# Performance work log

Measured on AMD Instinct MI355X. Metric: run time of the kernel, lower is better.

## Reference

```python
import jax, jax.numpy as jnp
import numpy as np

EPS_ANGLE = 1e-8   # eps in _cos_angle's F.normalize
EPS_NORM = 1e-12   # default F.normalize eps used for the similarity matrix
TOPK = 4
EXTRA_FRAMES = (1, 3, 5, 7)          # teacher-only frames
SHARED_TEACHER = (2, 4, 6)           # shared frames in teacher indexing
SHARED_STUDENT = (1, 2, 3)           # same frames in student indexing
W1 = W2 = W3 = 1.0


def _angle_cosines(ref, shared, sim):
    """Cosines of the 3 RKD angles for every (ref r, shared s, sim k) triplet.
    ref: [B,R,D], shared: [B,S,D], sim: [B,R,K,D]. Returns 3 arrays [B,R,S,K].
    Uses the dot-product expansion (u-v).(w-v) = uw - uv - vw + vv so the
    [B,R,S,K,D] difference tensors are never materialized (same math as the
    chunked torch loop)."""
    rr = jnp.sum(ref * ref, -1)                       # [B,R]
    ss = jnp.sum(shared * shared, -1)                 # [B,S]
    hh = jnp.sum(sim * sim, -1)                       # [B,R,K]
    sr = jnp.einsum('brd,bsd->brs', ref, shared)      # [B,R,S]
    rh = jnp.einsum('brd,brkd->brk', ref, sim)        # [B,R,K]
    sh = jnp.einsum('bsd,brkd->brsk', shared, sim)    # [B,R,S,K]
    rr_ = rr[:, :, None, None]
    ss_ = ss[:, None, :, None]
    hh_ = hh[:, :, None, :]
    sr_ = sr[..., None]
    rh_ = rh[:, :, None, :]
    n_sr = jnp.sqrt(jnp.maximum(ss_ - 2 * sr_ + rr_, 0.0))  # ||shared-ref||
    n_hr = jnp.sqrt(jnp.maximum(hh_ - 2 * rh_ + rr_, 0.0))  # ||sim-ref||
    n_sh = jnp.sqrt(jnp.maximum(ss_ - 2 * sh + hh_, 0.0))   # ||shared-sim||
    cl = lambda n: jnp.maximum(n, EPS_ANGLE)
    a1 = (sh - rh_ - sr_ + rr_) / (cl(n_sr) * cl(n_hr))  # angle at ref
    a2 = (sr_ - sh - rh_ + hh_) / (cl(n_hr) * cl(n_sh))  # angle at sim
    a3 = (rh_ - sr_ - sh + ss_) / (cl(n_sr) * cl(n_sh))  # angle at shared
    return a1, a2, a3


def _l2n(x, eps):
    return x / jnp.maximum(jnp.linalg.norm(x, axis=-1, keepdims=True), eps)


def setup_inputs() -> dict:
    key = jax.random.key(0)
    k1, k2, k3, k4 = jax.random.split(key, 4)
    B, P, D = 4, 1024, 1024
    return {
        'teacher_feats': jax.random.normal(k1, (B, 8, P, D), dtype=jnp.float32),
        'student_feats': jax.random.normal(k2, (B, 4, P, D), dtype=jnp.float32),
        'ref_perm': jax.random.randint(k3, (256,), 0, P),
        'shared_perm': jax.random.randint(k4, (256,), 0, P),
    }


def reference(teacher_feats, student_feats, ref_perm, shared_perm):
    B, St, P, D = teacher_feats.shape
    R = ref_perm.shape[0]
    S = shared_perm.shape[0]
    sg = jax.lax.stop_gradient

    ref_t = sg(teacher_feats[:, 0, ref_perm, :])        # [B,R,D]
    ref_s = student_feats[:, 0, ref_perm, :]            # [B,R,D]

    # teacher-only (extra) frames, concatenated along patch dim -> [B,4P,D]
    extra_t = sg(teacher_feats[:, jnp.array(EXTRA_FRAMES), :, :]).reshape(B, len(EXTRA_FRAMES) * P, D)
    sim = jnp.einsum('brd,bed->bre', _l2n(ref_t, EPS_NORM), _l2n(extra_t, EPS_NORM))
    _, topk_idx = jax.lax.top_k(sim, TOPK)              # [B,R,K]
    sim_high = jax.vmap(lambda e, i: e[i])(extra_t, topk_idx)  # [B,R,K,D]
    sim_high = sg(sim_high)

    s1 = s2 = s3 = jnp.float32(0.0)
    for ti, si in zip(SHARED_TEACHER, SHARED_STUDENT):
        sh_t = sg(teacher_feats[:, ti, shared_perm, :])
        sh_s = student_feats[:, si, shared_perm, :]
        a1t, a2t, a3t = _angle_cosines(ref_t, sh_t, sim_high)
        a1s, a2s, a3s = _angle_cosines(ref_s, sh_s, sim_high)
        s1 = s1 + jnp.sum(jnp.abs(a1s - sg(a1t)))
        s2 = s2 + jnp.sum(jnp.abs(a2s - sg(a2t)))
        s3 = s3 + jnp.sum(jnp.abs(a3s - sg(a3t)))

    total_elements = len(SHARED_TEACHER) * B * R * S * TOPK
    loss = (W1 * s1 + W2 * s2 + W3 * s3) / total_elements
    return loss
```

## Files before the change

kernel.cpp:

```cpp
#include <hip/hip_runtime.h>
#include <float.h>

#define BB 4
#define PP 1024
#define DD 1024
#define RR 256
#define SSZ 256
#define KT 4
#define EE 4096
#define NPAIR 3

typedef float  f32x4  __attribute__((ext_vector_type(4)));
typedef short  short8 __attribute__((ext_vector_type(8)));

#define MFMA16(a,b,c) __builtin_amdgcn_mfma_f32_16x16x32_bf16((a),(b),(c),0,0,0)

#define OFF_NE    ((size_t)0)
#define OFF_RR_T  ((size_t)16384)
#define OFF_RR_S  ((size_t)17408)
#define OFF_HH    ((size_t)18432)
#define OFF_RH_T  ((size_t)22528)
#define OFF_RH_S  ((size_t)26624)
#define OFF_SS_T  ((size_t)30720)
#define OFF_SS_S  ((size_t)33792)
#define OFF_TOPK  ((size_t)36864)
#define OFF_ACC   ((size_t)40960)
#define OFF_CAND  ((size_t)45056)
#define FLOAT_END ((size_t)569344)

#define U_REF_T ((size_t)0)
#define U_REF_S ((size_t)2097152)
#define U_SIMH  ((size_t)4194304)
#define U_SH_T  ((size_t)8388608)
#define U_SH_S  ((size_t)11534336)
#define U_EXT   ((size_t)14680064)

__device__ inline float block_sum256(float v, float* sb) {
  v += __shfl_down(v, 32); v += __shfl_down(v, 16);
  v += __shfl_down(v, 8);  v += __shfl_down(v, 4);
  v += __shfl_down(v, 2);  v += __shfl_down(v, 1);
  int lane = threadIdx.x & 63, wid = threadIdx.x >> 6;
  if (lane == 0) sb[wid] = v;
  __syncthreads();
  float r = 0.f;
  if (threadIdx.x < 4) r = sb[threadIdx.x];
  r += __shfl_down(r, 2); r += __shfl_down(r, 1);
  __syncthreads();
  return r;
}

__device__ inline float dot4(const float4& a, const float4& b) {
  return a.x*b.x + a.y*b.y + a.z*b.z + a.w*b.w;
}

__device__ inline unsigned short bhi(float x) {
  unsigned u = __float_as_uint(x);
  return (unsigned short)((u + 0x7fffu + ((u >> 16) & 1u)) >> 16);
}
__device__ inline ushort4 h4of(float4 f) {
  return make_ushort4(bhi(f.x), bhi(f.y), bhi(f.z), bhi(f.w));
}

__device__ inline size_t wofs(size_t base, int R, int t) {
  int rr = R & 15;
  int ss = ((t >> 1) & 3) ^ ((rr >> 1) & 3);
  return base + (size_t)(R >> 4)*16384 + (size_t)(t >> 3)*512
       + rr*32 + ss*8 + (t & 1)*4;
}

__global__ __launch_bounds__(256) void k_prep(const float* __restrict__ T,
                                              const float* __restrict__ Sf,
                                              const int* __restrict__ ref_perm,
                                              const int* __restrict__ shared_perm,
                                              float* __restrict__ ws) {
  __shared__ float sb[4];
  ushort* uws = (ushort*)(ws + FLOAT_END);
  int blk = blockIdx.x;
  int t = threadIdx.x;
  if (blk < 1024) {
    int b = blk >> 8, r = blk & 255;
    int pos = ref_perm[r];
    const float4* ts = (const float4*)(T  + ((size_t)(b*8 + 0)*PP + pos)*DD);
    const float4* sv = (const float4*)(Sf + ((size_t)(b*4 + 0)*PP + pos)*DD);
    float4 a = ts[t], c = sv[t];
    int R = b*RR + r;
    *(ushort4*)(uws + wofs(U_REF_T, R, t)) = h4of(a);
    *(ushort4*)(uws + wofs(U_REF_S, R, t)) = h4of(c);
    float r1 = block_sum256(dot4(a, a), sb);
    float r2 = block_sum256(dot4(c, c), sb);
    if (t == 0) {
      ws[OFF_RR_T + R] = r1;
      ws[OFF_RR_S + R] = r2;
    }
  } else if (blk < 17408) {
    int i = blk - 1024;
    int b = i >> 12, e = i & 4095;
    int f = 1 + 2*(e >> 10);
    int pos = e & 1023;
    const float4* src = (const float4*)(T + ((size_t)(b*8 + f)*PP + pos)*DD);
    float4 a = src[t];
    *(ushort4*)(uws + wofs(U_EXT, b*EE + e, t)) = h4of(a);
    float tot = block_sum256(dot4(a, a), sb);
    if (t == 0) ws[OFF_NE + (size_t)b*EE + e] = fmaxf(sqrtf(tot), 1e-12f);
  } else {
    int idx = blk - 17408;
    int p = idx / (BB*SSZ);
    int b = (idx / SSZ) % BB;
    int s = idx % SSZ;
    int pos = shared_perm[s];
    int ti = 2*(p + 1), si = p + 1;
    const float4* tr = (const float4*)(T  + ((size_t)(b*8 + ti)*PP + pos)*DD);
    const float4* sr = (const float4*)(Sf + ((size_t)(b*4 + si)*PP + pos)*DD);
    float4 a = tr[t], c = sr[t];
    *(ushort4*)(uws + wofs(U_SH_T, idx, t)) = h4of(a);
    *(ushort4*)(uws + wofs(U_SH_S, idx, t)) = h4of(c);
    float r1 = block_sum256(dot4(a, a), sb);
    float r2 = block_sum256(dot4(c, c), sb);
    if (t == 0) { ws[OFF_SS_T + idx] = r1; ws[OFF_SS_S + idx] = r2; }
  }
}

__global__ __launch_bounds__(256) void k_sim(float* __restrict__ ws) {
  __shared__ float simv[4][16][68];
  const ushort* uws = (const ushort*)(ws + FLOAT_END);
  int d = blockIdx.x;
  int u8 = d & 7, q = d >> 3;
  int b = u8 >> 1, eh = u8 & 1;
  int eb = eh*32 + (q >> 2);
  int rgq = q & 3;
  int tid = threadIdx.x;
  int w = tid >> 6, lane = tid & 63;
  int rg = rgq*4 + w;
  int r0 = rg*16, e0 = eb*64;
  int l15 = lane & 15, lq = (lane >> 4) & 3;
  int laneoff = l15*32 + ((lq ^ ((l15 >> 1) & 3)))*8;

  const ushort* pA = uws + U_REF_T + ((size_t)((b*RR + r0) >> 4))*16384 + laneoff;
  const ushort* pB0 = uws + U_EXT + ((size_t)((b*EE + e0) >> 4) + 0)*16384 + laneoff;
  const ushort* pB1 = uws + U_EXT + ((size_t)((b*EE + e0) >> 4) + 1)*16384 + laneoff;
  const ushort* pB2 = uws + U_EXT + ((size_t)((b*EE + e0) >> 4) + 2)*16384 + laneoff;
  const ushort* pB3 = uws + U_EXT + ((size_t)((b*EE + e0) >> 4) + 3)*16384 + laneoff;

  f32x4 acc[4];
#pragma unroll
  for (int j = 0; j < 4; ++j) acc[j] = (f32x4){0.f, 0.f, 0.f, 0.f};

#pragma unroll 4
  for (int c = 0; c < 32; ++c) {
    int o = c*512;
    short8 ah = *(const short8*)(pA + o);
    short8 b0 = *(const short8*)(pB0 + o);
    short8 b1 = *(const short8*)(pB1 + o);
    short8 b2 = *(const short8*)(pB2 + o);
    short8 b3 = *(const short8*)(pB3 + o);
    acc[0] = MFMA16(ah, b0, acc[0]);
    acc[1] = MFMA16(ah, b1, acc[1]);
    acc[2] = MFMA16(ah, b2, acc[2]);
    acc[3] = MFMA16(ah, b3, acc[3]);
  }

  float invs[4];
#pragma unroll
  for (int j = 0; j < 4; ++j)
    invs[j] = 1.f / ws[OFF_NE + (size_t)b*EE + e0 + j*16 + l15];
#pragma unroll
  for (int j = 0; j < 4; ++j)
#pragma unroll
    for (int q2 = 0; q2 < 4; ++q2)
      simv[w][lq*4 + q2][j*16 + l15] = acc[j][q2] * invs[j];
  if (lane < 16) {
    float v[4] = {-FLT_MAX, -FLT_MAX, -FLT_MAX, -FLT_MAX};
    int ix[4] = {0x7fffffff, 0x7fffffff, 0x7fffffff, 0x7fffffff};
#pragma unroll 1
    for (int e = 0; e < 64; ++e) {
      float f = simv[w][lane][e];
      if (f > v[3]) {
        int eg = e0 + e;
        if (f > v[0])      { v[3]=v[2]; ix[3]=ix[2]; v[2]=v[1]; ix[2]=ix[1]; v[1]=v[0]; ix[1]=ix[0]; v[0]=f; ix[0]=eg; }
        else if (f > v[1]) { v[3]=v[2]; ix[3]=ix[2]; v[2]=v[1]; ix[2]=ix[1]; v[1]=f; ix[1]=eg; }
        else if (f > v[2]) { v[3]=v[2]; ix[3]=ix[2]; v[2]=f; ix[2]=eg; }
        else               { v[3]=f; ix[3]=eg; }
      }
    }
    float2* cand = (float2*)(ws + OFF_CAND);
    size_t base = (((size_t)(b*RR + r0 + lane))*64 + eb)*4;
#pragma unroll
    for (int k = 0; k < 4; ++k)
      cand[base + k] = make_float2(v[k], __int_as_float(ix[k]));
  }
}

__global__ __launch_bounds__(256) void k_topk2(float* __restrict__ ws) {
  __shared__ float rv[256];
  __shared__ int   ri[256];
  __shared__ int   winIdx;
  int br = blockIdx.x;
  int tid = threadIdx.x;
  const float2* cand = (const float2*)(ws + OFF_CAND);
  float2 c = cand[(size_t)br*256 + tid];
  float v = c.x;
  int idx = __float_as_int(c.y);
  int* outi = (int*)(ws + OFF_TOPK) + (size_t)br*KT;
  for (int k = 0; k < KT; ++k) {
    rv[tid] = v; ri[tid] = idx;
    __syncthreads();
    for (int off = 128; off > 0; off >>= 1) {
      if (tid < off) {
        float v2 = rv[tid+off]; int i2 = ri[tid+off];
        if (v2 > rv[tid] || (v2 == rv[tid] && i2 < ri[tid])) { rv[tid] = v2; ri[tid] = i2; }
      }
      __syncthreads();
    }
    if (tid == 0) { outi[k] = ri[0]; winIdx = ri[0]; }
    __syncthreads();
    if (idx == winIdx) v = -FLT_MAX;
    __syncthreads();
  }
}

__global__ __launch_bounds__(256) void k_gather_high(const float* __restrict__ T,
                                                     const float* __restrict__ Sf,
                                                     const int* __restrict__ ref_perm,
                                                     float* __restrict__ ws) {
  __shared__ float sb[4];
  int idx = blockIdx.x;
  int e = ((const int*)(ws + OFF_TOPK))[idx];
  int b = idx >> 10;
  int r = (idx >> 2) & 255;
  int rpos = ref_perm[r];
  const float4* src = (const float4*)(T + ((size_t)(b*8 + 1 + 2*(e >> 10))*PP + (e & 1023))*DD);
  const float4* rt  = (const float4*)(T  + ((size_t)(b*8 + 0)*PP + rpos)*DD);
  const float4* rs  = (const float4*)(Sf + ((size_t)(b*4 + 0)*PP + rpos)*DD);
  ushort* uws = (ushort*)(ws + FLOAT_END);
  int t = threadIdx.x;
  float4 h = src[t];
  *(ushort4*)(uws + wofs(U_SIMH, idx, t)) = h4of(h);
  float4 a = rt[t], c = rs[t];
  float r1 = block_sum256(dot4(h, h), sb);
  float r2 = block_sum256(dot4(h, a), sb);
  float r3 = block_sum256(dot4(h, c), sb);
  if (t == 0) { ws[OFF_HH + idx] = r1; ws[OFF_RH_T + idx] = r2; ws[OFF_RH_S + idx] = r3; }
}

__global__ __launch_bounds__(256) void k_main(float* __restrict__ ws,
                                              double* __restrict__ acc_out) {
  __shared__ float Ct[4][80][17];
  __shared__ float Cs2[4][80][17];
  __shared__ float sb[4];
  const ushort* uws = (const ushort*)(ws + FLOAT_END);

  int d = blockIdx.x;
  int u8 = d & 7, q = d >> 3;
  int b = u8 >> 1, rhalf = u8 & 1;
  int p = q >> 4;
  int rem = q & 15;
  int s32i = rem >> 1, rq = rem & 1;
  int tid = threadIdx.x;
  int w = tid >> 6, lane = tid & 63;
  int z = p*4 + b;
  int r16i = rhalf*8 + rq*4 + w;
  int r0 = r16i*16, s0 = s32i*32;

  int l15 = lane & 15, lq = (lane >> 4) & 3;
  int laneoff = l15*32 + ((lq ^ ((l15 >> 1) & 3)))*8;

  const ushort* pa0; const ushort* pa1; const ushort* pa2; const ushort* pa3;
  const ushort* prt; const ushort* prs;
  const ushort* pbt0; const ushort* pbt1; const ushort* pbs0; const ushort* pbs1;
  {
    size_t gs = (size_t)((b*RR + r0) >> 2);
    pa0 = uws + U_SIMH + (gs + 0)*16384 + laneoff;
    pa1 = uws + U_SIMH + (gs + 1)*16384 + laneoff;
    pa2 = uws + U_SIMH + (gs + 2)*16384 + laneoff;
    pa3 = uws + U_SIMH + (gs + 3)*16384 + laneoff;
    size_t gr = (size_t)((b*RR + r0) >> 4);
    prt = uws + U_REF_T + gr*16384 + laneoff;
    prs = uws + U_REF_S + gr*16384 + laneoff;
    size_t gh = (size_t)((z*SSZ + s0) >> 4);
    pbt0 = uws + U_SH_T + (gh + 0)*16384 + laneoff;
    pbt1 = uws + U_SH_T + (gh + 1)*16384 + laneoff;
    pbs0 = uws + U_SH_S + (gh + 0)*16384 + laneoff;
    pbs1 = uws + U_SH_S + (gh + 1)*16384 + laneoff;
  }

  f32x4 aT0[2], aT1[2], aT2[2], aT3[2], aRT[2];
  f32x4 aS0[2], aS1[2], aS2[2], aS3[2], aRS[2];
#pragma unroll
  for (int h = 0; h < 2; ++h) {
    aT0[h] = aT1[h] = aT2[h] = aT3[h] = aRT[h] = (f32x4){0.f,0.f,0.f,0.f};
    aS0[h] = aS1[h] = aS2[h] = aS3[h] = aRS[h] = (f32x4){0.f,0.f,0.f,0.f};
  }

#pragma unroll 2
  for (int c = 0; c < 32; ++c) {
    int o = c*512;
    short8 bt0 = *(const short8*)(pbt0 + o);
    short8 bt1 = *(const short8*)(pbt1 + o);
    short8 bs0 = *(const short8*)(pbs0 + o);
    short8 bs1 = *(const short8*)(pbs1 + o);
    short8 a0 = *(const short8*)(pa0 + o);
    short8 a1 = *(const short8*)(pa1 + o);
    short8 a2 = *(const short8*)(pa2 + o);
    short8 a3 = *(const short8*)(pa3 + o);
    short8 rt = *(const short8*)(prt + o);
    short8 rs = *(const short8*)(prs + o);
    aT0[0] = MFMA16(a0, bt0, aT0[0]);  aT0[1] = MFMA16(a0, bt1, aT0[1]);
    aT1[0] = MFMA16(a1, bt0, aT1[0]);  aT1[1] = MFMA16(a1, bt1, aT1[1]);
    aT2[0] = MFMA16(a2, bt0, aT2[0]);  aT2[1] = MFMA16(a2, bt1, aT2[1]);
    aT3[0] = MFMA16(a3, bt0, aT3[0]);  aT3[1] = MFMA16(a3, bt1, aT3[1]);
    aRT[0] = MFMA16(rt, bt0, aRT[0]);  aRT[1] = MFMA16(rt, bt1, aRT[1]);
    aS0[0] = MFMA16(a0, bs0, aS0[0]);  aS0[1] = MFMA16(a0, bs1, aS0[1]);
    aS1[0] = MFMA16(a1, bs0, aS1[0]);  aS1[1] = MFMA16(a1, bs1, aS1[1]);
    aS2[0] = MFMA16(a2, bs0, aS2[0]);  aS2[1] = MFMA16(a2, bs1, aS2[1]);
    aS3[0] = MFMA16(a3, bs0, aS3[0]);  aS3[1] = MFMA16(a3, bs1, aS3[1]);
    aRS[0] = MFMA16(rs, bs0, aRS[0]);  aRS[1] = MFMA16(rs, bs1, aRS[1]);
  }

  int rl = lane >> 2, sg = lane & 3;
  int r = r0 + rl;
  float rrt = ws[OFF_RR_T + b*RR + r];
  float rrs = ws[OFF_RR_S + b*RR + r];
  float hhk[4], rhtk[4], rhsk[4], ihr_t[4], ihr_s[4];
#pragma unroll
  for (int k = 0; k < 4; ++k) {
    int idx = (b*RR + r)*KT + k;
    hhk[k]  = ws[OFF_HH + idx];
    rhtk[k] = ws[OFF_RH_T + idx];
    rhsk[k] = ws[OFF_RH_S + idx];
    float nt = sqrtf(fmaxf(hhk[k] - 2.f*rhtk[k] + rrt, 0.f));
    float ns = sqrtf(fmaxf(hhk[k] - 2.f*rhsk[k] + rrs, 0.f));
    ihr_t[k] = 1.f / fmaxf(nt, 1e-8f);
    ihr_s[k] = 1.f / fmaxf(ns, 1e-8f);
  }

  float local = 0.f;
#pragma unroll
  for (int h = 0; h < 2; ++h) {
#pragma unroll
    for (int q2 = 0; q2 < 4; ++q2) {
      int rg = lq*4 + q2;
      Ct[w][ 0 + rg][l15] = aT0[h][q2];
      Ct[w][16 + rg][l15] = aT1[h][q2];
      Ct[w][32 + rg][l15] = aT2[h][q2];
      Ct[w][48 + rg][l15] = aT3[h][q2];
      Ct[w][64 + rg][l15] = aRT[h][q2];
      Cs2[w][ 0 + rg][l15] = aS0[h][q2];
      Cs2[w][16 + rg][l15] = aS1[h][q2];
      Cs2[w][32 + rg][l15] = aS2[h][q2];
      Cs2[w][48 + rg][l15] = aS3[h][q2];
      Cs2[w][64 + rg][l15] = aRS[h][q2];
    }
#pragma unroll
    for (int j = 0; j < 4; ++j) {
      int sl = sg*4 + j;
      int sidx = z*SSZ + s0 + h*16 + sl;
      float sst = ws[OFF_SS_T + sidx];
      float sss = ws[OFF_SS_S + sidx];
      float srt = Ct[w][64 + rl][sl];
      float srs = Cs2[w][64 + rl][sl];
      float isr_t = 1.f / fmaxf(sqrtf(fmaxf(sst - 2.f*srt + rrt, 0.f)), 1e-8f);
      float isr_s = 1.f / fmaxf(sqrtf(fmaxf(sss - 2.f*srs + rrs, 0.f)), 1e-8f);
#pragma unroll
      for (int k = 0; k < 4; ++k) {
        float sht = Ct[w][rl*4 + k][sl];
        float shs = Cs2[w][rl*4 + k][sl];
        float ish_t = 1.f / fmaxf(sqrtf(fmaxf(sst - 2.f*sht + hhk[k], 0.f)), 1e-8f);
        float ish_s = 1.f / fmaxf(sqrtf(fmaxf(sss - 2.f*shs + hhk[k], 0.f)), 1e-8f);
        float a1t = (sht - rhtk[k] - srt + rrt) * (isr_t * ihr_t[k]);
        float a2t = (srt - sht - rhtk[k] + hhk[k]) * (ihr_t[k] * ish_t);
        float a3t = (rhtk[k] - srt - sht + sst) * (isr_t * ish_t);
        float a1s = (shs - rhsk[k] - srs + rrs) * (isr_s * ihr_s[k]);
        float a2s = (srs - shs - rhsk[k] + hhk[k]) * (ihr_s[k] * ish_s);
        float a3s = (rhsk[k] - srs - shs + sss) * (isr_s * ish_s);
        local += fabsf(a1s - a1t) + fabsf(a2s - a2t) + fabsf(a3s - a3t);
      }
    }
  }
  float tot = block_sum256(local, sb);
  if (tid == 0) atomicAdd(acc_out, (double)tot);
}

__global__ void k_final(const double* __restrict__ acc, float* __restrict__ out) {
  out[0] = (float)(acc[0] / 3145728.0);
}

extern "C" void kernel_launch(void* const* d_in, const int* in_sizes, int n_in,
                              void* d_out, int out_size, void* d_ws, size_t ws_size,
                              hipStream_t stream) {
  const float* T  = (const float*)d_in[0];
  const float* Sf = (const float*)d_in[1];
  const int* ref_perm    = (const int*)d_in[2];
  const int* shared_perm = (const int*)d_in[3];
  float* ws = (float*)d_ws;
  double* acc = (double*)(ws + OFF_ACC);

  hipMemsetAsync(acc, 0, sizeof(double), stream);
  k_prep<<<20480, 256, 0, stream>>>(T, Sf, ref_perm, shared_perm, ws);
  k_sim<<<1024, 256, 0, stream>>>(ws);
  k_topk2<<<BB*RR, 256, 0, stream>>>(ws);
  k_gather_high<<<BB*RR*KT, 256, 0, stream>>>(T, Sf, ref_perm, ws);
  k_main<<<384, 256, 0, stream>>>(ws, acc);
  k_final<<<1, 1, 0, stream>>>(acc, (float*)d_out);
}
```

Measured before the change: 123.0 us.

## Fuse top-k selection with high-sim gather and rebalance main kernel to 512 blocks

Merges the top-k reduction kernel and the gather kernel into one, so each block picks its 4 winners and then gathers the rows with one wave per selected row, using wave shuffles instead of block reductions. This removes a kernel launch and the global round-trip of top-k indices. Separately, k_main is remapped from 384 blocks of 4 waves to 512 blocks of 3 waves, with the same total work spread across more blocks to improve CU balance. The block reduction is replaced by shuffles plus a 3-entry shared sum.

```diff
diff --git a/kernel.cpp b/kernel.cpp
--- a/kernel.cpp
+++ b/kernel.cpp
@@ -190,16 +190,20 @@
   }
 }
 
-__global__ __launch_bounds__(256) void k_topk2(float* __restrict__ ws) {
+__global__ __launch_bounds__(256) void k_select(const float* __restrict__ T,
+                                                const float* __restrict__ Sf,
+                                                const int* __restrict__ ref_perm,
+                                                float* __restrict__ ws) {
   __shared__ float rv[256];
   __shared__ int   ri[256];
   __shared__ int   winIdx;
+  __shared__ int   sel[4];
   int br = blockIdx.x;
   int tid = threadIdx.x;
   const float2* cand = (const float2*)(ws + OFF_CAND);
-  float2 c = cand[(size_t)br*256 + tid];
-  float v = c.x;
-  int idx = __float_as_int(c.y);
+  float2 c0 = cand[(size_t)br*256 + tid];
+  float v = c0.x;
+  int idx = __float_as_int(c0.y);
   int* outi = (int*)(ws + OFF_TOPK) + (size_t)br*KT;
   for (int k = 0; k < KT; ++k) {
     rv[tid] = v; ri[tid] = idx;
@@ -211,54 +215,66 @@
       }
       __syncthreads();
     }
-    if (tid == 0) { outi[k] = ri[0]; winIdx = ri[0]; }
+    if (tid == 0) { outi[k] = ri[0]; winIdx = ri[0]; sel[k] = ri[0]; }
     __syncthreads();
     if (idx == winIdx) v = -FLT_MAX;
     __syncthreads();
   }
-}
-
-__global__ __launch_bounds__(256) void k_gather_high(const float* __restrict__ T,
-                                                     const float* __restrict__ Sf,
-                                                     const int* __restrict__ ref_perm,
-                                                     float* __restrict__ ws) {
-  __shared__ float sb[4];
-  int idx = blockIdx.x;
-  int e = ((const int*)(ws + OFF_TOPK))[idx];
-  int b = idx >> 10;
-  int r = (idx >> 2) & 255;
+
+  int b = br >> 8, r = br & 255;
+  int g = tid >> 6, lane = tid & 63;
+  int e = sel[g];
   int rpos = ref_perm[r];
   const float4* src = (const float4*)(T + ((size_t)(b*8 + 1 + 2*(e >> 10))*PP + (e & 1023))*DD);
   const float4* rt  = (const float4*)(T  + ((size_t)(b*8 + 0)*PP + rpos)*DD);
   const float4* rs  = (const float4*)(Sf + ((size_t)(b*4 + 0)*PP + rpos)*DD);
   ushort* uws = (ushort*)(ws + FLOAT_END);
-  int t = threadIdx.x;
-  float4 h = src[t];
-  *(ushort4*)(uws + wofs(U_SIMH, idx, t)) = h4of(h);
-  float4 a = rt[t], c = rs[t];
-  float r1 = block_sum256(dot4(h, h), sb);
-  float r2 = block_sum256(dot4(h, a), sb);
-  float r3 = block_sum256(dot4(h, c), sb);
-  if (t == 0) { ws[OFF_HH + idx] = r1; ws[OFF_RH_T + idx] = r2; ws[OFF_RH_S + idx] = r3; }
-}
-
-__global__ __launch_bounds__(256) void k_main(float* __restrict__ ws,
+  int rowi = br*KT + g;
+  float hh = 0.f, rht = 0.f, rhs = 0.f;
+#pragma unroll
+  for (int i = 0; i < 4; ++i) {
+    int t4 = lane*4 + i;
+    float4 h = src[t4];
+    *(ushort4*)(uws + wofs(U_SIMH, rowi, t4)) = h4of(h);
+    float4 a = rt[t4], c = rs[t4];
+    hh  += dot4(h, h);
+    rht += dot4(h, a);
+    rhs += dot4(h, c);
+  }
+  hh  += __shfl_down(hh, 32);  hh  += __shfl_down(hh, 16);
+  hh  += __shfl_down(hh, 8);   hh  += __shfl_down(hh, 4);
+  hh  += __shfl_down(hh, 2);   hh  += __shfl_down(hh, 1);
+  rht += __shfl_down(rht, 32); rht += __shfl_down(rht, 16);
+  rht += __shfl_down(rht, 8);  rht += __shfl_down(rht, 4);
+  rht += __shfl_down(rht, 2);  rht += __shfl_down(rht, 1);
+  rhs += __shfl_down(rhs, 32); rhs += __shfl_down(rhs, 16);
+  rhs += __shfl_down(rhs, 8);  rhs += __shfl_down(rhs, 4);
+  rhs += __shfl_down(rhs, 2);  rhs += __shfl_down(rhs, 1);
+  if (lane == 0) {
+    ws[OFF_HH + rowi]   = hh;
+    ws[OFF_RH_T + rowi] = rht;
+    ws[OFF_RH_S + rowi] = rhs;
+  }
+}
+
+__global__ __launch_bounds__(192) void k_main(float* __restrict__ ws,
                                               double* __restrict__ acc_out) {
-  __shared__ float Ct[4][80][17];
-  __shared__ float Cs2[4][80][17];
-  __shared__ float sb[4];
+  __shared__ float Ct[3][80][17];
+  __shared__ float Cs2[3][80][17];
+  __shared__ float sb[3];
   const ushort* uws = (const ushort*)(ws + FLOAT_END);
 
   int d = blockIdx.x;
   int u8 = d & 7, q = d >> 3;
   int b = u8 >> 1, rhalf = u8 & 1;
-  int p = q >> 4;
-  int rem = q & 15;
-  int s32i = rem >> 1, rq = rem & 1;
   int tid = threadIdx.x;
   int w = tid >> 6, lane = tid & 63;
+  int t = q*3 + w;
+  int p = t >> 6;
+  int rem = t & 63;
+  int s32i = rem >> 3, r16q = rem & 7;
   int z = p*4 + b;
-  int r16i = rhalf*8 + rq*4 + w;
+  int r16i = rhalf*8 + r16q;
   int r0 = r16i*16, s0 = s32i*32;
 
   int l15 = lane & 15, lq = (lane >> 4) & 3;
@@ -376,8 +392,14 @@
       }
     }
   }
-  float tot = block_sum256(local, sb);
-  if (tid == 0) atomicAdd(acc_out, (double)tot);
+
+  float v = local;
+  v += __shfl_down(v, 32); v += __shfl_down(v, 16);
+  v += __shfl_down(v, 8);  v += __shfl_down(v, 4);
+  v += __shfl_down(v, 2);  v += __shfl_down(v, 1);
+  if (lane == 0) sb[w] = v;
+  __syncthreads();
+  if (tid == 0) atomicAdd(acc_out, (double)(sb[0] + sb[1] + sb[2]));
 }
 
 __global__ void k_final(const double* __restrict__ acc, float* __restrict__ out) {
@@ -397,8 +419,7 @@
   hipMemsetAsync(acc, 0, sizeof(double), stream);
   k_prep<<<20480, 256, 0, stream>>>(T, Sf, ref_perm, shared_perm, ws);
   k_sim<<<1024, 256, 0, stream>>>(ws);
-  k_topk2<<<BB*RR, 256, 0, stream>>>(ws);
-  k_gather_high<<<BB*RR*KT, 256, 0, stream>>>(T, Sf, ref_perm, ws);
-  k_main<<<384, 256, 0, stream>>>(ws, acc);
+  k_select<<<BB*RR, 256, 0, stream>>>(T, Sf, ref_perm, ws);
+  k_main<<<512, 192, 0, stream>>>(ws, acc);
   k_final<<<1, 1, 0, stream>>>(acc, (float*)d_out);
 }
```

Result: faster. 118.1 us (median of 2 runs) (-4.0%).
